# Performance work log

Hardware: AMD Instinct MI355X
Metric: run time of the kernel (lower is better)

## Reference

```python
import jax, jax.numpy as jnp
import numpy as np

N = 50_000
E = 800_000
H = 128
EDGE_DIM = 1
NEG = 0.01  # leaky_relu slope used throughout AttentiveFP


def _lrelu(x):
    return jnp.where(x >= 0, x, NEG * x)


def _seg_softmax(logits, seg, num_segments):
    # numerically stable softmax over edges grouped by target segment
    m = jax.ops.segment_max(logits, seg, num_segments=num_segments)
    e = jnp.exp(logits - m[seg])
    s = jax.ops.segment_sum(e, seg, num_segments=num_segments)
    return e / s[seg]


def _gru(x, h, Wih, Whh, bih, bhh):
    # torch.nn.GRUCell: gates ordered r, z, n
    gi = x @ Wih.T + bih
    gh = h @ Whh.T + bhh
    ir, iz, inn = jnp.split(gi, 3, axis=-1)
    hr, hz, hn = jnp.split(gh, 3, axis=-1)
    r = jax.nn.sigmoid(ir + hr)
    z = jax.nn.sigmoid(iz + hz)
    n = jnp.tanh(inn + r * hn)
    return (1.0 - z) * n + z * h


def setup_inputs() -> dict:
    key = jax.random.key(0)
    ks = jax.random.split(key, 32)
    def rn(k, shape, s=0.1):
        return jax.random.normal(k, shape, dtype=jnp.float32) * s
    return {
        "node_attr": jax.random.normal(ks[0], (N, 1), dtype=jnp.float32),
        "edge_index": jax.random.randint(ks[1], (2, E), 0, N),
        "edge_attr": jax.random.normal(ks[2], (E, EDGE_DIM), dtype=jnp.float32),
        "W_lin1": rn(ks[3], (H, 1)), "b_lin1": rn(ks[4], (H,)),
        "gate_W1": rn(ks[5], (H, H + EDGE_DIM)), "gate_W2": rn(ks[6], (H, H)),
        "gate_att_l": rn(ks[7], (H,)), "gate_att_r": rn(ks[8], (H,)),
        "gate_b": rn(ks[9], (H,)),
        "gru1_Wih": rn(ks[10], (3 * H, H)), "gru1_Whh": rn(ks[11], (3 * H, H)),
        "gru1_bih": rn(ks[12], (3 * H,)), "gru1_bhh": rn(ks[13], (3 * H,)),
        "atom_W": rn(ks[14], (H, H)), "atom_att_src": rn(ks[15], (H,)),
        "atom_att_dst": rn(ks[16], (H,)), "atom_b": rn(ks[17], (H,)),
        "gru2_Wih": rn(ks[18], (3 * H, H)), "gru2_Whh": rn(ks[19], (3 * H, H)),
        "gru2_bih": rn(ks[20], (3 * H,)), "gru2_bhh": rn(ks[21], (3 * H,)),
        "mol_W": rn(ks[22], (H, H)), "mol_att_src": rn(ks[23], (H,)),
        "mol_att_dst": rn(ks[24], (H,)), "mol_b": rn(ks[25], (H,)),
        "grum_Wih": rn(ks[26], (3 * H, H)), "grum_Whh": rn(ks[27], (3 * H, H)),
        "grum_bih": rn(ks[28], (3 * H,)), "grum_bhh": rn(ks[29], (3 * H,)),
    }


def _forward(node_attr, edge_index, edge_attr, W_lin1, b_lin1, gate_W1, gate_W2,
             gate_att_l, gate_att_r, gate_b, gru1_Wih, gru1_Whh, gru1_bih, gru1_bhh,
             atom_W, atom_att_src, atom_att_dst, atom_b, gru2_Wih, gru2_Whh,
             gru2_bih, gru2_bhh, mol_W, mol_att_src, mol_att_dst, mol_b,
             grum_Wih, grum_Whh, grum_bih, grum_bhh):
    src, dst = edge_index[0], edge_index[1]  # j -> i (aggregate at dst)
    n = node_attr.shape[0]
    # lin1 + leaky_relu
    x = _lrelu(node_attr @ W_lin1.T + b_lin1)  # [N,H]
    # --- GATEConv (edge-featured attention) ---
    xj = _lrelu(jnp.concatenate([x[src], edge_attr], axis=-1) @ gate_W1.T)  # [E,H]
    alpha = _lrelu(xj @ gate_att_l + (x @ gate_att_r)[dst])  # [E]
    alpha = _seg_softmax(alpha, dst, n)
    h = jax.ops.segment_sum((x[src] @ gate_W2.T) * alpha[:, None], dst, num_segments=n) + gate_b
    h = jax.nn.elu(h)
    x = jax.nn.relu(_gru(h, x, gru1_Wih, gru1_Whh, gru1_bih, gru1_bhh))
    # --- GATConv layer (num_layers=2 -> one) ---
    xt = x @ atom_W.T  # [N,H]
    a = _lrelu((xt * atom_att_src).sum(-1)[src] + (xt * atom_att_dst).sum(-1)[dst])
    a = _seg_softmax(a, dst, n)
    h = jax.ops.segment_sum(xt[src] * a[:, None], dst, num_segments=n) + atom_b
    h = jax.nn.elu(h)
    x = jax.nn.relu(_gru(h, x, gru2_Wih, gru2_Whh, gru2_bih, gru2_bhh))
    # --- molecule embedding: batch = zeros -> single graph; num_timesteps=1 ---
    batch = jnp.zeros((n,), dtype=jnp.int32)
    out = jax.nn.relu(jax.ops.segment_sum(x, batch, num_segments=1))  # [1,H]
    xs = x @ mol_W.T          # node-side transform (shared lin)
    outs = out @ mol_W.T      # graph-side transform
    a = _lrelu((xs * mol_att_src).sum(-1) + (outs * mol_att_dst).sum(-1)[batch])
    a = _seg_softmax(a, batch, 1)
    h = jax.nn.elu(jax.ops.segment_sum(xs * a[:, None], batch, num_segments=1) + mol_b)
    out = jax.nn.relu(_gru(h, out, grum_Wih, grum_Whh, grum_bih, grum_bhh))
    return out  # [1, H] graph embedding (layer1 output, out_channels=hidden)


def reference(node_attr, edge_index, edge_attr, W_lin1, b_lin1, gate_W1, gate_W2,
              gate_att_l, gate_att_r, gate_b, gru1_Wih, gru1_Whh, gru1_bih, gru1_bhh,
              atom_W, atom_att_src, atom_att_dst, atom_b, gru2_Wih, gru2_Whh,
              gru2_bih, gru2_bhh, mol_W, mol_att_src, mol_att_dst, mol_b,
              grum_Wih, grum_Whh, grum_bih, grum_bhh):
    return _forward(node_attr, edge_index, edge_attr, W_lin1, b_lin1, gate_W1,
                    gate_W2, gate_att_l, gate_att_r, gate_b, gru1_Wih, gru1_Whh,
                    gru1_bih, gru1_bhh, atom_W, atom_att_src, atom_att_dst, atom_b,
                    gru2_Wih, gru2_Whh, gru2_bih, gru2_bhh, mol_W, mol_att_src,
                    mol_att_dst, mol_b, grum_Wih, grum_Whh, grum_bih, grum_bhh)
```

## Files before the change

kernel.cpp:

```cpp
#include <hip/hip_runtime.h>
#include <math.h>

#define H 128
#define NEGS 0.01f

typedef __attribute__((ext_vector_type(8))) short short8;
typedef __attribute__((ext_vector_type(4))) float f32x4;

__device__ __forceinline__ float lrelu(float x){ return x >= 0.f ? x : NEGS*x; }
__device__ __forceinline__ float eluf(float x){ return x > 0.f ? x : expf(x)-1.f; }
__device__ __forceinline__ float sigm(float x){ return 1.f/(1.f+expf(-x)); }
__device__ __forceinline__ float wred(float v){
  #pragma unroll
  for (int off = 32; off > 0; off >>= 1) v += __shfl_xor(v, off, 64);
  return v;
}
__device__ __forceinline__ float wredmax(float v){
  #pragma unroll
  for (int off = 32; off > 0; off >>= 1) v = fmaxf(v, __shfl_xor(v, off, 64));
  return v;
}
__device__ __forceinline__ unsigned fenc(float f){
  unsigned u = __float_as_uint(f);
  return (u & 0x80000000u) ? ~u : (u | 0x80000000u);
}
__device__ __forceinline__ float fdec(unsigned v){
  return __uint_as_float((v & 0x80000000u) ? (v ^ 0x80000000u) : ~v);
}
__device__ __forceinline__ unsigned short f2bf(float f){
  unsigned u = __float_as_uint(f);
  u += 0x7fffu + ((u >> 16) & 1u);
  return (unsigned short)(u >> 16);
}
__device__ __forceinline__ float bf2f(unsigned short h){
  return __uint_as_float(((unsigned)h) << 16);
}
__device__ __forceinline__ float rdlane(float v, int l){
  return __int_as_float(__builtin_amdgcn_readlane(__float_as_int(v), l));
}
__device__ __forceinline__ int rdlanei(int v, int l){
  return __builtin_amdgcn_readlane(v, l);
}

__global__ void k_castall(const float* __restrict__ gW1, const float* __restrict__ gW2,
                          const float* __restrict__ atomW, const float* __restrict__ molW,
                          const float* __restrict__ g1ih, const float* __restrict__ g1hh,
                          const float* __restrict__ g2ih, const float* __restrict__ g2hh,
                          unsigned short* __restrict__ dst){
  int idx = blockIdx.x*256 + threadIdx.x;
  const float* src; int ld = 128; int off;
  if      (idx <  16384){ src = gW1;  ld = 129; off = idx; }
  else if (idx <  32768){ src = gW2;  off = idx -  16384; }
  else if (idx <  49152){ src = atomW;off = idx -  32768; }
  else if (idx <  65536){ src = molW; off = idx -  49152; }
  else if (idx < 114688){ src = g1ih; off = idx -  65536; }
  else if (idx < 163840){ src = g1hh; off = idx - 114688; }
  else if (idx < 212992){ src = g2ih; off = idx - 163840; }
  else                  { src = g2hh; off = idx - 212992; }
  int r = off >> 7, c = off & 127;
  dst[idx] = f2bf(src[r*ld + c]);
}

__global__ void k_node_init_rd(const float* __restrict__ na, const float* __restrict__ wl,
                               const float* __restrict__ bl, const float* __restrict__ attr,
                               unsigned short* __restrict__ x, float* __restrict__ rdot, int n){
  int i = blockIdx.x*4 + (threadIdx.x >> 6);
  int lane = threadIdx.x & 63;
  if (i >= n) return;
  float nav = na[i];
  float v0 = lrelu(nav*wl[2*lane]   + bl[2*lane]);
  float v1 = lrelu(nav*wl[2*lane+1] + bl[2*lane+1]);
  ushort2 o; o.x = f2bf(v0); o.y = f2bf(v1);
  *(ushort2*)&x[(size_t)i*H + 2*lane] = o;
  float d = bf2f(o.x)*attr[2*lane] + bf2f(o.y)*attr[2*lane+1];
  d = wred(d);
  if (lane == 0) rdot[i] = d;
}

__global__ __launch_bounds__(256)
void k_gemm_mfma(const unsigned short* __restrict__ X, const unsigned short* __restrict__ Wbf,
                 unsigned short* __restrict__ Y, int n, int ldy,
                 const float* __restrict__ v1, const float* __restrict__ v2,
                 float* __restrict__ o1, float* __restrict__ o2){
  int w = threadIdx.x >> 6;
  int l = threadIdx.x & 63;
  int i0 = blockIdx.x*64 + w*16;
  int mbase = blockIdx.y*128;
  int row = l & 15;
  int kg  = l >> 4;
  f32x4 acc[8];
  #pragma unroll
  for (int c = 0; c < 8; ++c) acc[c] = (f32x4){0.f,0.f,0.f,0.f};
  int ai = i0 + row;
  bool av = (ai < n);
  #pragma unroll
  for (int ks = 0; ks < 4; ++ks){
    int koff = ks*32 + kg*8;
    short8 a = av ? *(const short8*)&X[(size_t)ai*H + koff]
                  : (short8){0,0,0,0,0,0,0,0};
    #pragma unroll
    for (int c = 0; c < 8; ++c){
      short8 b = *(const short8*)&Wbf[(size_t)(mbase + c*16 + row)*H + koff];
      acc[c] = __builtin_amdgcn_mfma_f32_16x16x32_bf16(a, b, acc[c], 0, 0, 0);
    }
  }
  #pragma unroll
  for (int c = 0; c < 8; ++c){
    #pragma unroll
    for (int r = 0; r < 4; ++r){
      int i = i0 + kg*4 + r;
      if (i < n) Y[(size_t)i*ldy + mbase + c*16 + row] = f2bf(acc[c][r]);
    }
  }
  if (v1){
    #pragma unroll
    for (int r = 0; r < 4; ++r){
      float p1 = 0.f, p2 = 0.f;
      #pragma unroll
      for (int c = 0; c < 8; ++c){
        p1 += acc[c][r]*v1[c*16 + row];
        if (v2) p2 += acc[c][r]*v2[c*16 + row];
      }
      #pragma unroll
      for (int off = 1; off < 16; off <<= 1){
        p1 += __shfl_xor(p1, off, 64);
        if (v2) p2 += __shfl_xor(p2, off, 64);
      }
      int i = i0 + kg*4 + r;
      if (row == 0 && i < n){ o1[i] = p1; if (v2) o2[i] = p2; }
    }
  }
}

__global__ void k_gru_combine(const unsigned short* __restrict__ gi, const unsigned short* __restrict__ gh,
                              const float* __restrict__ bih, const float* __restrict__ bhh,
                              unsigned short* __restrict__ x, int n){
  int idx = blockIdx.x*blockDim.x + threadIdx.x;
  if (idx >= n*64) return;
  int i = idx >> 6, t = (idx & 63)*2;
  const unsigned short* gir = gi + (size_t)i*384;
  const unsigned short* ghr = gh + (size_t)i*384;
  ushort2 uir = *(const ushort2*)&gir[t];
  ushort2 uiz = *(const ushort2*)&gir[t+128];
  ushort2 uin = *(const ushort2*)&gir[t+256];
  ushort2 uhr = *(const ushort2*)&ghr[t];
  ushort2 uhz = *(const ushort2*)&ghr[t+128];
  ushort2 uhn = *(const ushort2*)&ghr[t+256];
  ushort2 ux  = *(const ushort2*)&x[(size_t)i*H + t];
  float2 b_ir = *(const float2*)&bih[t], b_iz = *(const float2*)&bih[t+128], b_in = *(const float2*)&bih[t+256];
  float2 b_hr = *(const float2*)&bhh[t], b_hz = *(const float2*)&bhh[t+128], b_hn = *(const float2*)&bhh[t+256];
  ushort2 o;
  {
    float r = sigm(bf2f(uir.x)+b_ir.x + bf2f(uhr.x)+b_hr.x);
    float z = sigm(bf2f(uiz.x)+b_iz.x + bf2f(uhz.x)+b_hz.x);
    float nn = tanhf(bf2f(uin.x)+b_in.x + r*(bf2f(uhn.x)+b_hn.x));
    o.x = f2bf(fmaxf((1.f-z)*nn + z*bf2f(ux.x), 0.f));
  }
  {
    float r = sigm(bf2f(uir.y)+b_ir.y + bf2f(uhr.y)+b_hr.y);
    float z = sigm(bf2f(uiz.y)+b_iz.y + bf2f(uhz.y)+b_hz.y);
    float nn = tanhf(bf2f(uin.y)+b_in.y + r*(bf2f(uhn.y)+b_hn.y));
    o.y = f2bf(fmaxf((1.f-z)*nn + z*bf2f(ux.y), 0.f));
  }
  *(ushort2*)&x[(size_t)i*H + t] = o;
}

__global__ void k_hist(const int* __restrict__ key, int* __restrict__ deg, int ne){
  int e = blockIdx.x*blockDim.x + threadIdx.x;
  if (e < ne) atomicAdd(&deg[key[e]], 1);
}
__global__ void k_scan1(const int* __restrict__ deg, int* __restrict__ bsum, int n){
  __shared__ int sd[256];
  int i = blockIdx.x*256 + threadIdx.x;
  sd[threadIdx.x] = (i < n) ? deg[i] : 0;
  __syncthreads();
  for (int s = 128; s > 0; s >>= 1){
    if (threadIdx.x < s) sd[threadIdx.x] += sd[threadIdx.x+s];
    __syncthreads();
  }
  if (threadIdx.x == 0) bsum[blockIdx.x] = sd[0];
}
__global__ void k_scan2(int* __restrict__ bsum, int nb){
  __shared__ int sd[256];
  int t = threadIdx.x;
  int v = (t < nb) ? bsum[t] : 0;
  sd[t] = v;
  __syncthreads();
  for (int off = 1; off < 256; off <<= 1){
    int u = (t >= off) ? sd[t-off] : 0;
    __syncthreads();
    sd[t] += u;
    __syncthreads();
  }
  if (t < nb) bsum[t] = sd[t] - v;
}
__global__ void k_scan3(const int* __restrict__ deg, const int* __restrict__ boff,
                        int* __restrict__ rowptr, int* __restrict__ cursor, int n){
  __shared__ int sd[256];
  int t = threadIdx.x;
  int i = blockIdx.x*256 + t;
  int v = (i < n) ? deg[i] : 0;
  sd[t] = v;
  __syncthreads();
  for (int off = 1; off < 256; off <<= 1){
    int u = (t >= off) ? sd[t-off] : 0;
    __syncthreads();
    sd[t] += u;
    __syncthreads();
  }
  int excl = sd[t] - v + boff[blockIdx.x];
  if (i < n){
    rowptr[i] = excl; cursor[i] = excl;
    if (i == n-1) rowptr[n] = excl + v;
  }
}
__global__ void k_fill_dst(const int* __restrict__ src, const int* __restrict__ dst,
                           const float* __restrict__ ea, int* __restrict__ cursor,
                           int2* __restrict__ sea, int ne){
  int e = blockIdx.x*blockDim.x + threadIdx.x;
  if (e >= ne) return;
  int pos = atomicAdd(&cursor[dst[e]], 1);
  sea[pos] = make_int2(src[e], __float_as_int(ea[e]));
}

__global__ void k_pack_gate(const float* __restrict__ gateW1, float* __restrict__ w1col){
  int t = threadIdx.x;
  if (t < H) w1col[t] = gateW1[t*129 + 128];
}

__global__ __launch_bounds__(256)
void k_edge_logit_gate(const unsigned short* __restrict__ xW1, const float* __restrict__ w1col,
                       const float* __restrict__ attl, const int2* __restrict__ sea,
                       float* __restrict__ logit_s, int ne){
  int tid = threadIdx.x;
  int j = blockIdx.x*32 + (tid >> 3);
  int g = tid & 7;
  if (j >= ne) return;
  int2 se = sea[j];
  int s = se.x;
  float eav = __int_as_float(se.y);
  const unsigned short* xr = &xW1[(size_t)s*H + g*16];
  short8 r0 = *(const short8*)xr;
  short8 r1 = *(const short8*)(xr + 8);
  float acc = 0.f;
  #pragma unroll
  for (int kk = 0; kk < 8; ++kk)
    acc += lrelu(bf2f((unsigned short)r0[kk]) + eav*w1col[g*16 + kk]) * attl[g*16 + kk];
  #pragma unroll
  for (int kk = 0; kk < 8; ++kk)
    acc += lrelu(bf2f((unsigned short)r1[kk]) + eav*w1col[g*16 + 8 + kk]) * attl[g*16 + 8 + kk];
  #pragma unroll
  for (int off = 1; off < 8; off <<= 1) acc += __shfl_xor(acc, off, 64);
  if (g == 0) logit_s[j] = acc;
}

__global__ void k_node_agg(const int* __restrict__ rowptr, const int2* __restrict__ sea,
                           const float* __restrict__ logit_s, const float* __restrict__ rdot,
                           const unsigned short* __restrict__ val, const float* __restrict__ bias,
                           unsigned short* __restrict__ hbuf, int n){
  int i = blockIdx.x*4 + (threadIdx.x >> 6);
  int lane = threadIdx.x & 63;
  if (i >= n) return;
  int b = rowptr[i], e1 = rowptr[i+1];
  float rd = rdot[i];
  float m = -1e30f;
  for (int j = b+lane; j < e1; j += 64) m = fmaxf(m, lrelu(logit_s[j] + rd));
  m = wredmax(m);
  float s = 0.f, ax = 0.f, ay = 0.f;
  for (int c0 = b; c0 < e1; c0 += 64){
    int cnt = min(64, e1 - c0);
    float wv = 0.f; int snv = 0;
    if (lane < cnt){
      snv = sea[c0 + lane].x;
      wv = expf(lrelu(logit_s[c0 + lane] + rd) - m);
    }
    s += wred(wv);
    int j = 0;
    for (; j+8 <= cnt; j += 8){
      #pragma unroll
      for (int u = 0; u < 8; ++u){
        float wq = rdlane(wv, j+u);
        int sq = rdlanei(snv, j+u);
        ushort2 v = *(const ushort2*)&val[(size_t)sq*H + 2*lane];
        ax += bf2f(v.x)*wq; ay += bf2f(v.y)*wq;
      }
    }
    for (; j < cnt; ++j){
      float wq = rdlane(wv, j);
      int sq = rdlanei(snv, j);
      ushort2 v = *(const ushort2*)&val[(size_t)sq*H + 2*lane];
      ax += bf2f(v.x)*wq; ay += bf2f(v.y)*wq;
    }
  }
  float inv = (s > 0.f) ? 1.f/s : 0.f;
  ushort2 o;
  o.x = f2bf(eluf(bias[2*lane]   + ax*inv));
  o.y = f2bf(eluf(bias[2*lane+1] + ay*inv));
  *(ushort2*)&hbuf[(size_t)i*H + 2*lane] = o;
}

__global__ void k_node_agg_gat(const int* __restrict__ rowptr, const int2* __restrict__ sea,
                               const float* __restrict__ ssrc, const float* __restrict__ sdst,
                               const unsigned short* __restrict__ val, const float* __restrict__ bias,
                               unsigned short* __restrict__ hbuf, int n){
  int i = blockIdx.x*4 + (threadIdx.x >> 6);
  int lane = threadIdx.x & 63;
  if (i >= n) return;
  int b = rowptr[i], e1 = rowptr[i+1];
  float sdi = sdst[i];
  float m = -1e30f;
  for (int j = b+lane; j < e1; j += 64) m = fmaxf(m, lrelu(ssrc[sea[j].x] + sdi));
  m = wredmax(m);
  float s = 0.f, ax = 0.f, ay = 0.f;
  for (int c0 = b; c0 < e1; c0 += 64){
    int cnt = min(64, e1 - c0);
    float wv = 0.f; int snv = 0;
    if (lane < cnt){
      snv = sea[c0 + lane].x;
      wv = expf(lrelu(ssrc[snv] + sdi) - m);
    }
    s += wred(wv);
    int j = 0;
    for (; j+8 <= cnt; j += 8){
      #pragma unroll
      for (int u = 0; u < 8; ++u){
        float wq = rdlane(wv, j+u);
        int sq = rdlanei(snv, j+u);
        ushort2 v = *(const ushort2*)&val[(size_t)sq*H + 2*lane];
        ax += bf2f(v.x)*wq; ay += bf2f(v.y)*wq;
      }
    }
    for (; j < cnt; ++j){
      float wq = rdlane(wv, j);
      int sq = rdlanei(snv, j);
      ushort2 v = *(const ushort2*)&val[(size_t)sq*H + 2*lane];
      ax += bf2f(v.x)*wq; ay += bf2f(v.y)*wq;
    }
  }
  float inv = (s > 0.f) ? 1.f/s : 0.f;
  ushort2 o;
  o.x = f2bf(eluf(bias[2*lane]   + ax*inv));
  o.y = f2bf(eluf(bias[2*lane+1] + ay*inv));
  *(ushort2*)&hbuf[(size_t)i*H + 2*lane] = o;
}

__global__ void k_colsum(const unsigned short* __restrict__ x, float* __restrict__ outraw,
                         int n, int chunk){
  int t = threadIdx.x;
  int start = blockIdx.x*chunk;
  int end = min(start + chunk, n);
  float s0 = 0.f, s1 = 0.f;
  for (int i = start; i < end; ++i){
    ushort2 v = *(const ushort2*)&x[(size_t)i*H + 2*t];
    s0 += bf2f(v.x); s1 += bf2f(v.y);
  }
  if (start < end){ atomicAdd(&outraw[2*t], s0); atomicAdd(&outraw[2*t+1], s1); }
}
__global__ void k_mol_prep(const float* __restrict__ outraw, const float* __restrict__ molW,
                           const float* __restrict__ attdst, float* __restrict__ hidvec,
                           float* __restrict__ cdst){
  __shared__ float hs[128];
  __shared__ float red[128];
  int t = threadIdx.x;
  float hv = fmaxf(outraw[t], 0.f);
  hs[t] = hv; hidvec[t] = hv;
  __syncthreads();
  float o = 0.f;
  for (int k = 0; k < 128; ++k) o += hs[k]*molW[t*128+k];
  red[t] = o * attdst[t];
  __syncthreads();
  for (int s = 64; s > 0; s >>= 1){
    if (t < s) red[t] += red[t+s];
    __syncthreads();
  }
  if (t == 0) cdst[0] = red[0];
}
__global__ void k_mol_logit(float* __restrict__ a, const float* __restrict__ cdst,
                            unsigned* __restrict__ gmax, int n){
  int i = blockIdx.x*blockDim.x + threadIdx.x;
  int lane = threadIdx.x & 63;
  float l = -1e30f;
  if (i < n){
    l = lrelu(a[i] + cdst[0]);
    a[i] = l;
  }
  float mm = wredmax(l);
  if (lane == 0) atomicMax(gmax, fenc(mm));
}
__global__ void k_mol_exp(float* __restrict__ a, const unsigned* __restrict__ gmax,
                          float* __restrict__ gsum, int n){
  int i = blockIdx.x*blockDim.x + threadIdx.x;
  int lane = threadIdx.x & 63;
  float gm = fdec(gmax[0]);
  float ex = 0.f;
  if (i < n){ ex = expf(a[i] - gm); a[i] = ex; }
  float s = wred(ex);
  if (lane == 0) atomicAdd(gsum, s);
}
__global__ void k_mol_acc(const unsigned short* __restrict__ xs, const float* __restrict__ a,
                          float* __restrict__ num, int n, int chunk){
  int t = threadIdx.x;
  int start = blockIdx.x*chunk;
  int end = min(start + chunk, n);
  float s0 = 0.f, s1 = 0.f;
  for (int i = start; i < end; ++i){
    float ai = a[i];
    ushort2 v = *(const ushort2*)&xs[(size_t)i*H + 2*t];
    s0 += bf2f(v.x)*ai; s1 += bf2f(v.y)*ai;
  }
  if (start < end){ atomicAdd(&num[2*t], s0); atomicAdd(&num[2*t+1], s1); }
}
__global__ void k_mol_final(const float* __restrict__ num, const float* __restrict__ gsum,
                            const float* __restrict__ molb, const float* __restrict__ hidvec,
                            const float* __restrict__ Wih, const float* __restrict__ Whh,
                            const float* __restrict__ bih, const float* __restrict__ bhh,
                            float* __restrict__ out){
  __shared__ float hv[128], hd[128];
  int t = threadIdx.x;
  hv[t] = eluf(num[t]/gsum[0] + molb[t]);
  hd[t] = hidvec[t];
  __syncthreads();
  float gr = bih[t], gz = bih[t+128], gn = bih[t+256];
  float hr = bhh[t], hz = bhh[t+128], hn = bhh[t+256];
  for (int k = 0; k < 128; ++k){
    float h = hv[k], d = hd[k];
    gr += h*Wih[t*128+k];       gz += h*Wih[(t+128)*128+k]; gn += h*Wih[(t+256)*128+k];
    hr += d*Whh[t*128+k];       hz += d*Whh[(t+128)*128+k]; hn += d*Whh[(t+256)*128+k];
  }
  float r = sigm(gr+hr), z = sigm(gz+hz);
  float nn = tanhf(gn + r*hn);
  float o = (1.f-z)*nn + z*hd[t];
  out[t] = fmaxf(o, 0.f);
}

extern "C" void kernel_launch(void* const* d_in, const int* in_sizes, int n_in,
                              void* d_out, int out_size, void* d_ws, size_t ws_size,
                              hipStream_t stream){
  const float* node_attr = (const float*)d_in[0];
  const int*   eidx      = (const int*)d_in[1];
  const float* eattr     = (const float*)d_in[2];
  const float* W_lin1    = (const float*)d_in[3];
  const float* b_lin1    = (const float*)d_in[4];
  const float* gate_W1   = (const float*)d_in[5];
  const float* gate_W2   = (const float*)d_in[6];
  const float* gate_att_l= (const float*)d_in[7];
  const float* gate_att_r= (const float*)d_in[8];
  const float* gate_b    = (const float*)d_in[9];
  const float* g1_Wih    = (const float*)d_in[10];
  const float* g1_Whh    = (const float*)d_in[11];
  const float* g1_bih    = (const float*)d_in[12];
  const float* g1_bhh    = (const float*)d_in[13];
  const float* atom_W    = (const float*)d_in[14];
  const float* atom_as   = (const float*)d_in[15];
  const float* atom_ad   = (const float*)d_in[16];
  const float* atom_b    = (const float*)d_in[17];
  const float* g2_Wih    = (const float*)d_in[18];
  const float* g2_Whh    = (const float*)d_in[19];
  const float* g2_bih    = (const float*)d_in[20];
  const float* g2_bhh    = (const float*)d_in[21];
  const float* mol_W     = (const float*)d_in[22];
  const float* mol_as    = (const float*)d_in[23];
  const float* mol_ad    = (const float*)d_in[24];
  const float* mol_b     = (const float*)d_in[25];
  const float* gm_Wih    = (const float*)d_in[26];
  const float* gm_Whh    = (const float*)d_in[27];
  const float* gm_bih    = (const float*)d_in[28];
  const float* gm_bhh    = (const float*)d_in[29];

  const int n  = in_sizes[0];
  const int ne = in_sizes[1] / 2;
  const int* src = eidx;
  const int* dst = eidx + ne;

  const size_t NH = (size_t)n * H;
  unsigned short* us = (unsigned short*)d_ws;
  unsigned short* x_bf = us;
  unsigned short* t0   = us + NH;
  unsigned short* t1   = us + 2*NH;
  unsigned short* hb   = us + 3*NH;
  unsigned short* gi   = us + 4*NH;
  unsigned short* gh   = us + 7*NH;
  float* fb = (float*)(us + 10*NH);
  float* rdot = fb;
  float* ssrc = rdot + n;
  float* sdst = ssrc + n;
  float* logit_s = sdst + n;
  int* deg    = (int*)(logit_s + ne);
  int* cursor = deg + n;
  int* rowptr = cursor + n;
  int* bsum   = rowptr + n + 1;
  size_t ioff = (size_t)(bsum + 256 - (int*)d_ws);
  ioff = (ioff + 1) & ~(size_t)1;
  int2* sea  = (int2*)((int*)d_ws + ioff);
  float* outraw = (float*)(sea + ne);
  float* hidvec = outraw + 128;
  float* cdstp  = hidvec + 128;
  unsigned* gmax = (unsigned*)(cdstp + 1);
  float* gsum   = (float*)gmax + 1;
  float* numv   = gsum + 1;
  float* w1col  = numv + 128 + 1;
  unsigned short* wp = (unsigned short*)(w1col + 128);
  unsigned short* gW1bf  = wp;
  unsigned short* gW2bf  = gW1bf  + 128*H;
  unsigned short* atomWbf= gW2bf  + 128*H;
  unsigned short* molWbf = atomWbf+ 128*H;
  unsigned short* g1ihbf = molWbf + 128*H;
  unsigned short* g1hhbf = g1ihbf + 384*H;
  unsigned short* g2ihbf = g1hhbf + 384*H;
  unsigned short* g2hhbf = g2ihbf + 384*H;

  const int nb64       = (n + 63)/64;
  const int nwave4     = (n + 3)/4;
  const int e32_blocks = (ne + 31)/32;
  const int ethr       = (ne + 255)/256;
  const int nthr       = (n + 255)/256;
  const int nb         = (n + 255)/256;
  const int chunk      = (n + 255)/256;
  const int gru_blocks = (n*64 + 255)/256;

  k_castall<<<1024,256,0,stream>>>(gate_W1, gate_W2, atom_W, mol_W,
                                   g1_Wih, g1_Whh, g2_Wih, g2_Whh, wp);
  k_pack_gate<<<1,128,0,stream>>>(gate_W1, w1col);
  k_node_init_rd<<<nwave4,256,0,stream>>>(node_attr, W_lin1, b_lin1, gate_att_r, x_bf, rdot, n);
  hipMemsetAsync(deg, 0, (size_t)n*4, stream);
  k_hist<<<ethr,256,0,stream>>>(dst, deg, ne);
  k_scan1<<<nb,256,0,stream>>>(deg, bsum, n);
  k_scan2<<<1,256,0,stream>>>(bsum, nb);
  k_scan3<<<nb,256,0,stream>>>(deg, bsum, rowptr, cursor, n);
  k_fill_dst<<<ethr,256,0,stream>>>(src, dst, eattr, cursor, sea, ne);

  k_gemm_mfma<<<dim3(nb64,1),256,0,stream>>>(x_bf, gW1bf, t0, n, H,
                                             nullptr, nullptr, nullptr, nullptr);
  k_gemm_mfma<<<dim3(nb64,1),256,0,stream>>>(x_bf, gW2bf, t1, n, H,
                                             nullptr, nullptr, nullptr, nullptr);
  k_edge_logit_gate<<<e32_blocks,256,0,stream>>>(t0, w1col, gate_att_l, sea, logit_s, ne);
  k_node_agg<<<nwave4,256,0,stream>>>(rowptr, sea, logit_s, rdot, t1, gate_b, hb, n);
  k_gemm_mfma<<<dim3(nb64,3),256,0,stream>>>(hb,   g1ihbf, gi, n, 384,
                                             nullptr, nullptr, nullptr, nullptr);
  k_gemm_mfma<<<dim3(nb64,3),256,0,stream>>>(x_bf, g1hhbf, gh, n, 384,
                                             nullptr, nullptr, nullptr, nullptr);
  k_gru_combine<<<gru_blocks,256,0,stream>>>(gi, gh, g1_bih, g1_bhh, x_bf, n);

  k_gemm_mfma<<<dim3(nb64,1),256,0,stream>>>(x_bf, atomWbf, t0, n, H,
                                             atom_as, atom_ad, ssrc, sdst);
  k_node_agg_gat<<<nwave4,256,0,stream>>>(rowptr, sea, ssrc, sdst, t0, atom_b, hb, n);
  k_gemm_mfma<<<dim3(nb64,3),256,0,stream>>>(hb,   g2ihbf, gi, n, 384,
                                             nullptr, nullptr, nullptr, nullptr);
  k_gemm_mfma<<<dim3(nb64,3),256,0,stream>>>(x_bf, g2hhbf, gh, n, 384,
                                             nullptr, nullptr, nullptr, nullptr);
  k_gru_combine<<<gru_blocks,256,0,stream>>>(gi, gh, g2_bih, g2_bhh, x_bf, n);

  hipMemsetAsync(outraw, 0, 128*4, stream);
  hipMemsetAsync(gmax, 0, 4, stream);
  hipMemsetAsync(gsum, 0, 4, stream);
  hipMemsetAsync(numv, 0, 128*4, stream);
  k_colsum<<<256,64,0,stream>>>(x_bf, outraw, n, chunk);
  k_mol_prep<<<1,128,0,stream>>>(outraw, mol_W, mol_ad, hidvec, cdstp);
  k_gemm_mfma<<<dim3(nb64,1),256,0,stream>>>(x_bf, molWbf, t1, n, H,
                                             mol_as, nullptr, rdot, nullptr);
  k_mol_logit<<<nthr,256,0,stream>>>(rdot, cdstp, gmax, n);
  k_mol_exp<<<nthr,256,0,stream>>>(rdot, gmax, gsum, n);
  k_mol_acc<<<256,64,0,stream>>>(t1, rdot, numv, n, chunk);
  k_mol_final<<<1,128,0,stream>>>(numv, gsum, mol_b, hidvec,
                                  gm_Wih, gm_Whh, gm_bih, gm_bhh, (float*)d_out);
}
```

Before: 719.1 us.

## Fuse GRU input/hidden GEMMs with gate combine via LDS; merge gate GEMMs

Replaces the two 384-wide GRU GEMMs and the separate combine kernel with one 512-thread kernel. Four waves compute the input-side gates into LDS, four compute the hidden-side gates in registers, and the hidden-side waves apply the GRU update in place on x. This removes the gi/gh global round trips and two launches per GRU. The two gate-layer GEMMs are also merged into one launch by giving each grid-y slice its own output base, set by a new stride argument. In exchange each wave holds 24 accumulator tiles, so register pressure rises, and the kernel uses 48KB of LDS, which limits occupancy.

```diff
diff --git a/kernel.cpp b/kernel.cpp
--- a/kernel.cpp
+++ b/kernel.cpp
@@ -79,7 +79,7 @@
 
 __global__ __launch_bounds__(256)
 void k_gemm_mfma(const unsigned short* __restrict__ X, const unsigned short* __restrict__ Wbf,
-                 unsigned short* __restrict__ Y, int n, int ldy,
+                 unsigned short* __restrict__ Y, int n, int ldy, size_t ostride,
                  const float* __restrict__ v1, const float* __restrict__ v2,
                  float* __restrict__ o1, float* __restrict__ o2){
   int w = threadIdx.x >> 6;
@@ -104,12 +104,13 @@
       acc[c] = __builtin_amdgcn_mfma_f32_16x16x32_bf16(a, b, acc[c], 0, 0, 0);
     }
   }
+  unsigned short* Yb = Y + (size_t)blockIdx.y*ostride;
   #pragma unroll
   for (int c = 0; c < 8; ++c){
     #pragma unroll
     for (int r = 0; r < 4; ++r){
       int i = i0 + kg*4 + r;
-      if (i < n) Y[(size_t)i*ldy + mbase + c*16 + row] = f2bf(acc[c][r]);
+      if (i < n) Yb[(size_t)i*ldy + c*16 + row] = f2bf(acc[c][r]);
     }
   }
   if (v1){
@@ -132,37 +133,71 @@
   }
 }
 
-__global__ void k_gru_combine(const unsigned short* __restrict__ gi, const unsigned short* __restrict__ gh,
-                              const float* __restrict__ bih, const float* __restrict__ bhh,
-                              unsigned short* __restrict__ x, int n){
-  int idx = blockIdx.x*blockDim.x + threadIdx.x;
-  if (idx >= n*64) return;
-  int i = idx >> 6, t = (idx & 63)*2;
-  const unsigned short* gir = gi + (size_t)i*384;
-  const unsigned short* ghr = gh + (size_t)i*384;
-  ushort2 uir = *(const ushort2*)&gir[t];
-  ushort2 uiz = *(const ushort2*)&gir[t+128];
-  ushort2 uin = *(const ushort2*)&gir[t+256];
-  ushort2 uhr = *(const ushort2*)&ghr[t];
-  ushort2 uhz = *(const ushort2*)&ghr[t+128];
-  ushort2 uhn = *(const ushort2*)&ghr[t+256];
-  ushort2 ux  = *(const ushort2*)&x[(size_t)i*H + t];
-  float2 b_ir = *(const float2*)&bih[t], b_iz = *(const float2*)&bih[t+128], b_in = *(const float2*)&bih[t+256];
-  float2 b_hr = *(const float2*)&bhh[t], b_hz = *(const float2*)&bhh[t+128], b_hn = *(const float2*)&bhh[t+256];
-  ushort2 o;
-  {
-    float r = sigm(bf2f(uir.x)+b_ir.x + bf2f(uhr.x)+b_hr.x);
-    float z = sigm(bf2f(uiz.x)+b_iz.x + bf2f(uhz.x)+b_hz.x);
-    float nn = tanhf(bf2f(uin.x)+b_in.x + r*(bf2f(uhn.x)+b_hn.x));
-    o.x = f2bf(fmaxf((1.f-z)*nn + z*bf2f(ux.x), 0.f));
-  }
-  {
-    float r = sigm(bf2f(uir.y)+b_ir.y + bf2f(uhr.y)+b_hr.y);
-    float z = sigm(bf2f(uiz.y)+b_iz.y + bf2f(uhz.y)+b_hz.y);
-    float nn = tanhf(bf2f(uin.y)+b_in.y + r*(bf2f(uhn.y)+b_hn.y));
-    o.y = f2bf(fmaxf((1.f-z)*nn + z*bf2f(ux.y), 0.f));
-  }
-  *(ushort2*)&x[(size_t)i*H + t] = o;
+__global__ __launch_bounds__(512)
+void k_gru_fused2(const unsigned short* __restrict__ hb, unsigned short* __restrict__ x,
+                  const unsigned short* __restrict__ Wih, const unsigned short* __restrict__ Whh,
+                  const float* __restrict__ bih, const float* __restrict__ bhh, int n){
+  __shared__ unsigned short lgi[64*384];
+  int w = threadIdx.x >> 6;
+  int l = threadIdx.x & 63;
+  int side = w >> 2;
+  int mt = w & 3;
+  int i0 = blockIdx.x*64 + mt*16;
+  int row = l & 15, kg = l >> 4;
+  const unsigned short* A = side ? x : hb;
+  const unsigned short* W = side ? Whh : Wih;
+  f32x4 acc[24];
+  #pragma unroll
+  for (int c = 0; c < 24; ++c) acc[c] = (f32x4){0.f,0.f,0.f,0.f};
+  int ai = i0 + row;
+  bool av = (ai < n);
+  #pragma unroll
+  for (int ks = 0; ks < 4; ++ks){
+    int koff = ks*32 + kg*8;
+    short8 a = av ? *(const short8*)&A[(size_t)ai*H + koff]
+                  : (short8){0,0,0,0,0,0,0,0};
+    #pragma unroll
+    for (int c = 0; c < 24; ++c){
+      short8 b = *(const short8*)&W[(size_t)(c*16 + row)*H + koff];
+      acc[c] = __builtin_amdgcn_mfma_f32_16x16x32_bf16(a, b, acc[c], 0, 0, 0);
+    }
+  }
+  if (side == 0){
+    #pragma unroll
+    for (int c = 0; c < 24; ++c){
+      #pragma unroll
+      for (int r = 0; r < 4; ++r){
+        int node = mt*16 + kg*4 + r;
+        lgi[node*384 + c*16 + row] = f2bf(acc[c][r]);
+      }
+    }
+  }
+  __syncthreads();
+  if (side == 1){
+    #pragma unroll
+    for (int c = 0; c < 8; ++c){
+      int t = c*16 + row;
+      float bir = bih[t], biz = bih[t+128], bin = bih[t+256];
+      float bhr = bhh[t], bhz = bhh[t+128], bhn = bhh[t+256];
+      #pragma unroll
+      for (int r = 0; r < 4; ++r){
+        int node = mt*16 + kg*4 + r;
+        int i = blockIdx.x*64 + node;
+        if (i < n){
+          float gir = bf2f(lgi[node*384 + t      ]) + bir;
+          float giz = bf2f(lgi[node*384 + t + 128]) + biz;
+          float gin = bf2f(lgi[node*384 + t + 256]) + bin;
+          float ghr = acc[c][r]    + bhr;
+          float ghz = acc[c+8][r]  + bhz;
+          float ghn = acc[c+16][r] + bhn;
+          float rr = sigm(gir + ghr), z = sigm(giz + ghz);
+          float nn = tanhf(gin + rr*ghn);
+          float xo = (1.f - z)*nn + z*bf2f(x[(size_t)i*H + t]);
+          x[(size_t)i*H + t] = f2bf(fmaxf(xo, 0.f));
+        }
+      }
+    }
+  }
 }
 
 __global__ void k_hist(const int* __restrict__ key, int* __restrict__ deg, int ne){
@@ -478,9 +513,7 @@
   unsigned short* t0   = us + NH;
   unsigned short* t1   = us + 2*NH;
   unsigned short* hb   = us + 3*NH;
-  unsigned short* gi   = us + 4*NH;
-  unsigned short* gh   = us + 7*NH;
-  float* fb = (float*)(us + 10*NH);
+  float* fb = (float*)(us + 4*NH);
   float* rdot = fb;
   float* ssrc = rdot + n;
   float* sdst = ssrc + n;
@@ -516,7 +549,6 @@
   const int nthr       = (n + 255)/256;
   const int nb         = (n + 255)/256;
   const int chunk      = (n + 255)/256;
-  const int gru_blocks = (n*64 + 255)/256;
 
   k_castall<<<1024,256,0,stream>>>(gate_W1, gate_W2, atom_W, mol_W,
                                    g1_Wih, g1_Whh, g2_Wih, g2_Whh, wp);
@@ -529,26 +561,16 @@
   k_scan3<<<nb,256,0,stream>>>(deg, bsum, rowptr, cursor, n);
   k_fill_dst<<<ethr,256,0,stream>>>(src, dst, eattr, cursor, sea, ne);
 
-  k_gemm_mfma<<<dim3(nb64,1),256,0,stream>>>(x_bf, gW1bf, t0, n, H,
-                                             nullptr, nullptr, nullptr, nullptr);
-  k_gemm_mfma<<<dim3(nb64,1),256,0,stream>>>(x_bf, gW2bf, t1, n, H,
+  k_gemm_mfma<<<dim3(nb64,2),256,0,stream>>>(x_bf, gW1bf, t0, n, H, NH,
                                              nullptr, nullptr, nullptr, nullptr);
   k_edge_logit_gate<<<e32_blocks,256,0,stream>>>(t0, w1col, gate_att_l, sea, logit_s, ne);
   k_node_agg<<<nwave4,256,0,stream>>>(rowptr, sea, logit_s, rdot, t1, gate_b, hb, n);
-  k_gemm_mfma<<<dim3(nb64,3),256,0,stream>>>(hb,   g1ihbf, gi, n, 384,
-                                             nullptr, nullptr, nullptr, nullptr);
-  k_gemm_mfma<<<dim3(nb64,3),256,0,stream>>>(x_bf, g1hhbf, gh, n, 384,
-                                             nullptr, nullptr, nullptr, nullptr);
-  k_gru_combine<<<gru_blocks,256,0,stream>>>(gi, gh, g1_bih, g1_bhh, x_bf, n);
-
-  k_gemm_mfma<<<dim3(nb64,1),256,0,stream>>>(x_bf, atomWbf, t0, n, H,
+  k_gru_fused2<<<nb64,512,0,stream>>>(hb, x_bf, g1ihbf, g1hhbf, g1_bih, g1_bhh, n);
+
+  k_gemm_mfma<<<dim3(nb64,1),256,0,stream>>>(x_bf, atomWbf, t0, n, H, 0,
                                              atom_as, atom_ad, ssrc, sdst);
   k_node_agg_gat<<<nwave4,256,0,stream>>>(rowptr, sea, ssrc, sdst, t0, atom_b, hb, n);
-  k_gemm_mfma<<<dim3(nb64,3),256,0,stream>>>(hb,   g2ihbf, gi, n, 384,
-                                             nullptr, nullptr, nullptr, nullptr);
-  k_gemm_mfma<<<dim3(nb64,3),256,0,stream>>>(x_bf, g2hhbf, gh, n, 384,
-                                             nullptr, nullptr, nullptr, nullptr);
-  k_gru_combine<<<gru_blocks,256,0,stream>>>(gi, gh, g2_bih, g2_bhh, x_bf, n);
+  k_gru_fused2<<<nb64,512,0,stream>>>(hb, x_bf, g2ihbf, g2hhbf, g2_bih, g2_bhh, n);
 
   hipMemsetAsync(outraw, 0, 128*4, stream);
   hipMemsetAsync(gmax, 0, 4, stream);
@@ -556,7 +578,7 @@
   hipMemsetAsync(numv, 0, 128*4, stream);
   k_colsum<<<256,64,0,stream>>>(x_bf, outraw, n, chunk);
   k_mol_prep<<<1,128,0,stream>>>(outraw, mol_W, mol_ad, hidvec, cdstp);
-  k_gemm_mfma<<<dim3(nb64,1),256,0,stream>>>(x_bf, molWbf, t1, n, H,
+  k_gemm_mfma<<<dim3(nb64,1),256,0,stream>>>(x_bf, molWbf, t1, n, H, 0,
                                              mol_as, nullptr, rdot, nullptr);
   k_mol_logit<<<nthr,256,0,stream>>>(rdot, cdstp, gmax, n);
   k_mol_exp<<<nthr,256,0,stream>>>(rdot, gmax, gsum, n);
```

New measurement: 716.0 us. About the same (-0.4%).
